# Kernel optimization log

Measured on AMD Instinct MI355X. Metric: run time of the kernel, lower is better.

Reference implementation:

```python
import jax, jax.numpy as jnp
import numpy as np

# ---- static configuration (from init_kwargs) ----
K = 2                 # kernel_size -> (2K+1)^2 = 25 window offsets
WIN = 2 * K + 1       # 5
A = WIN * WIN         # 25 window slots (ir_in replicated A times)
MUL_IN = 16           # multiplicity of each input irrep (16x0e + 16x1e)
MUL_OUT = 32          # 32x0e + 32x1e
SH0 = float(1.0 / (2.0 * np.sqrt(np.pi)))       # Y_l=0, e3nn 'integral' norm
SH1 = float(np.sqrt(3.0 / (4.0 * np.pi)))       # Y_l=1 scale (normalize=False)
CG_110 = float(1.0 / np.sqrt(3.0))              # CG for 1x1 -> 0 (dot/sqrt3)
CG_111 = float(1.0 / np.sqrt(2.0))              # CG for 1x1 -> 1 (cross/sqrt2)
# path normalization: out irrep gets 1/sqrt(fan_in) with fan = n_paths * mul_u
A0 = float(1.0 / np.sqrt(2 * A * MUL_IN))       # 0e fed by paths (0e,0e)+(1e,1e) per slot
A1 = float(1.0 / np.sqrt(3 * A * MUL_IN))       # 1e fed by (0e,1e)+(1e,0e)+(1e,1e)


def setup_inputs() -> dict:
    key = jax.random.key(0)
    ks = jax.random.split(key, 7)
    feat = jax.random.normal(ks[0], (8, 64, 64, 64), dtype=jnp.float32)
    spin = jax.random.normal(ks[1], (8, 64, 64, 3), dtype=jnp.float32)
    wshape = (A, MUL_IN, MUL_OUT)  # one uvw block per window slot per path type
    W_000 = jax.random.normal(ks[2], wshape, dtype=jnp.float32)
    W_110 = jax.random.normal(ks[3], wshape, dtype=jnp.float32)
    W_011 = jax.random.normal(ks[4], wshape, dtype=jnp.float32)
    W_101 = jax.random.normal(ks[5], wshape, dtype=jnp.float32)
    W_111 = jax.random.normal(ks[6], wshape, dtype=jnp.float32)
    return {"feat": feat, "spin": spin, "W_000": W_000, "W_110": W_110,
            "W_011": W_011, "W_101": W_101, "W_111": W_111}


def spin2colsq2d(feat):
    # circular im2col: (N,Lx,Ly,F) -> (N,Lx,Ly,A,F)
    N, Lx, Ly, F = feat.shape
    p = jnp.pad(feat, ((0, 0), (K, K), (K, K), (0, 0)), mode='wrap')
    cols = [p[:, ix:ix + Lx, iy:iy + Ly, :]
            for ix in range(WIN) for iy in range(WIN)]
    return jnp.stack(cols, axis=3)


def reference(feat, spin, W_000, W_110, W_011, W_101, W_111):
    col = spin2colsq2d(feat)                                  # (N,Lx,Ly,A,64)
    x0 = col[..., :MUL_IN]                                    # (N,Lx,Ly,A,16) scalars
    x1 = col[..., MUL_IN:].reshape(col.shape[:-1] + (MUL_IN, 3))  # (N,Lx,Ly,A,16,3)
    # spherical harmonics of spin, l=0..1, normalize=False, integral norm
    sh1 = SH1 * spin                                          # (N,Lx,Ly,3)
    # ---- paths into 0e output ----
    dot = jnp.einsum('nxyaui,nxyi->nxyau', x1, sh1) * CG_110  # 1e x 1e -> 0e
    out0 = A0 * (SH0 * jnp.einsum('nxyau,auw->nxyw', x0, W_000)
                 + jnp.einsum('nxyau,auw->nxyw', dot, W_110))  # (N,Lx,Ly,32)
    # ---- paths into 1e output ----
    cross = jnp.cross(x1, sh1[..., None, None, :]) * CG_111   # 1e x 1e -> 1e
    out1 = A1 * (jnp.einsum('nxyau,nxyi,auw->nxywi', x0, sh1, W_011)
                 + SH0 * jnp.einsum('nxyaui,auw->nxywi', x1, W_101)
                 + jnp.einsum('nxyaui,auw->nxywi', cross, W_111))  # (N,Lx,Ly,32,3)
    out1 = out1.reshape(out1.shape[:-2] + (MUL_OUT * 3,))
    return jnp.concatenate([out0, out1], axis=-1)             # (N,Lx,Ly,128)
```

## Files before the change

kernel.cpp:

```cpp
#include <hip/hip_runtime.h>


typedef __attribute__((ext_vector_type(8))) short short8;
typedef __attribute__((ext_vector_type(16))) float f32x16;
typedef __attribute__((ext_vector_type(4))) float float4v;

typedef __attribute__((address_space(3))) unsigned char lds_u8_t;
typedef const __attribute__((address_space(1))) unsigned char g_u8_t;

#define FEATT_BYTES (8u * 64u * 64u * 64u * 2u)
#define BT_OFFSET   FEATT_BYTES

#define MFMA32(A, B, C) __builtin_amdgcn_mfma_f32_32x32x16_bf16(A, B, C, 0, 0, 0)

__device__ __forceinline__ unsigned short f2bf(float f) {
    unsigned int u = __float_as_uint(f);
    return (unsigned short)((u + 0x7FFFu + ((u >> 16) & 1u)) >> 16);
}

__global__ __launch_bounds__(256) void prep_kernel(
    const float* __restrict__ feat,
    const float* __restrict__ W000, const float* __restrict__ W110,
    const float* __restrict__ W011, const float* __restrict__ W101,
    const float* __restrict__ W111,
    unsigned char* __restrict__ ws)
{
    int tid = threadIdx.x;
    int b = blockIdx.x;
    if (b < 512) {
        __shared__ float sf[64][68];
        size_t base = (size_t)b * 4096;
        #pragma unroll
        for (int i = 0; i < 4; ++i) {
            int e = tid + i * 256;
            float4v v = *(const float4v*)(feat + base + (size_t)e * 4);
            int px = e >> 4;
            int c  = (e & 15) * 4;
            sf[px][c + 0] = v[0]; sf[px][c + 1] = v[1];
            sf[px][c + 2] = v[2]; sf[px][c + 3] = v[3];
        }
        __syncthreads();
        unsigned short* dst = (unsigned short*)ws + base;
        #pragma unroll
        for (int i = 0; i < 2; ++i) {
            int t = tid + i * 256;
            int s = t >> 6, px = t & 63;
            short8 o;
            #pragma unroll
            for (int j = 0; j < 8; ++j) {
                int chp = s * 8 + j;
                int c = (chp < 16) ? chp : (16 + 3 * ((chp - 16) & 15) + ((chp - 16) >> 4));
                o[j] = (short)f2bf(sf[px][c]);
            }
            *(short8*)(dst + s * 512 + px * 8) = o;
        }
    } else {
        int t = (b - 512) * 256 + tid;
        if (t >= 4000) return;
        int a = t / 160, colv = t - a * 160;
        int arr = colv >> 5, w = colv & 31;
        const float* Wp = (arr == 0) ? W000 : (arr == 1) ? W011
                        : (arr == 2) ? W110 : (arr == 3) ? W101 : W111;
        unsigned short tmp[16];
        #pragma unroll
        for (int k = 0; k < 16; ++k) tmp[k] = f2bf(Wp[a * 512 + k * 32 + w]);
        unsigned short* d = (unsigned short*)(ws + BT_OFFSET) + (size_t)t * 16;
        *(short8*)(d)     = *(short8*)(tmp);
        *(short8*)(d + 8) = *(short8*)(tmp + 8);
    }
}

__global__ __launch_bounds__(256, 3) void spinconv_mfma_kernel(
    const unsigned char* __restrict__ featT8,
    const unsigned char* __restrict__ bt,
    const float* __restrict__ spin,
    float* __restrict__ out)
{
    const float SH0f   = 0.28209479177387814f;
    const float CG110f = 0.5773502691896258f;
    const float CG111f = 0.7071067811865476f;
    const float A0f    = 0.035355339059327376f;
    const float A1f    = 0.028867513459481287f;

    __shared__ __align__(16) unsigned char fl[5 * 8 * 64 * 16];
    __shared__ float sbuf[2][16][64];
    __shared__ float s_lds[192];

    int tid = threadIdx.x;
    int b = blockIdx.x;
    int bid = ((b & 7) << 6) + (b >> 3);
    int x = bid & 63;

    int lane = tid & 63;
    int wv4 = tid >> 6;

    #pragma unroll
    for (int i = 0; i < 10; ++i) {
        int g = wv4 * 10 + i;
        int dx = g >> 3;
        int X = (x + dx + 62) & 63;
        const unsigned char* src = featT8
            + (size_t)(bid - x + X) * 8192 + (g & 7) * 1024 + lane * 16;
        __builtin_amdgcn_global_load_lds((g_u8_t*)src, (lds_u8_t*)(fl + g * 1024), 16, 0, 0);
    }
    if (tid < 192) {
        s_lds[tid] = 0.4886025119029199f * spin[(size_t)bid * 192 + tid];
    }
    __syncthreads();

    int pair = wv4 >> 1;
    int role = wv4 & 1;
    int col = lane & 31;
    int khalf = lane >> 5;
    int yb = pair << 5;
    int p0 = bid << 6;

    const unsigned char* bbase = bt + col * 32 + khalf * 16;
    float* rowbuf = (float*)fl;

    f32x16 zz;
    #pragma unroll
    for (int i = 0; i < 16; ++i) zz[i] = 0.f;

    f32x16 aS000 = zz, aS011 = zz, aV0 = zz, aV1 = zz, aV2 = zz;
    f32x16 aT0 = zz, aT1 = zz, aT2 = zz, aU0 = zz, aU1 = zz, aU2 = zz;

    if (role == 0) {
        short8 Bc0, Bc1, Bc2, Bn0, Bn1, Bn2;
        short8 Ax, Ac0, Ac1, Ac2, Nx, Nc0, Nc1, Nc2;

        auto loadB = [&](int a, short8& b0, short8& b1, short8& b2) {
            const unsigned char* p = bbase + a * 5120;
            b0 = *(const short8*)(p);
            b1 = *(const short8*)(p + 1024);
            b2 = *(const short8*)(p + 2048);
        };
        auto loadA = [&](int a, short8& ax, short8& c0, short8& c1, short8& c2) {
            int ix = a / 5;
            int iy = a - ix * 5;
            int yn = (yb + col + iy + 62) & 63;
            const unsigned char* ab = fl + ix * 8192 + yn * 16;
            ax = *(const short8*)(ab + (0 + khalf) * 1024);
            c0 = *(const short8*)(ab + (2 + khalf) * 1024);
            c1 = *(const short8*)(ab + (4 + khalf) * 1024);
            c2 = *(const short8*)(ab + (6 + khalf) * 1024);
        };

        loadB(0, Bc0, Bc1, Bc2);
        loadA(0, Ax, Ac0, Ac1, Ac2);
        #pragma unroll
        for (int ap = 0; ap < 25; ap += 2) {
            if (ap + 1 < 25) { loadB(ap + 1, Bn0, Bn1, Bn2); loadA(ap + 1, Nx, Nc0, Nc1, Nc2); }
            __builtin_amdgcn_s_setprio(1);
            aS000 = MFMA32(Ax,  Bc0, aS000);
            aS011 = MFMA32(Ax,  Bc1, aS011);
            aV0   = MFMA32(Ac0, Bc2, aV0);
            aV1   = MFMA32(Ac1, Bc2, aV1);
            aV2   = MFMA32(Ac2, Bc2, aV2);
            __builtin_amdgcn_s_setprio(0);
            if (ap + 1 < 25) {
                if (ap + 2 < 25) { loadB(ap + 2, Bc0, Bc1, Bc2); loadA(ap + 2, Ax, Ac0, Ac1, Ac2); }
                __builtin_amdgcn_s_setprio(1);
                aS000 = MFMA32(Nx,  Bn0, aS000);
                aS011 = MFMA32(Nx,  Bn1, aS011);
                aV0   = MFMA32(Nc0, Bn2, aV0);
                aV1   = MFMA32(Nc1, Bn2, aV1);
                aV2   = MFMA32(Nc2, Bn2, aV2);
                __builtin_amdgcn_s_setprio(0);
            }
        }
        #pragma unroll
        for (int r = 0; r < 16; ++r) sbuf[pair][r][lane] = aS011[r];
    } else {
        short8 Bc0, Bc1, Bn0, Bn1;
        short8 Ac0, Ac1, Ac2, Nc0, Nc1, Nc2;

        auto loadB = [&](int a, short8& b0, short8& b1) {
            const unsigned char* p = bbase + a * 5120;
            b0 = *(const short8*)(p + 3072);
            b1 = *(const short8*)(p + 4096);
        };
        auto loadA = [&](int a, short8& c0, short8& c1, short8& c2) {
            int ix = a / 5;
            int iy = a - ix * 5;
            int yn = (yb + col + iy + 62) & 63;
            const unsigned char* ab = fl + ix * 8192 + yn * 16;
            c0 = *(const short8*)(ab + (2 + khalf) * 1024);
            c1 = *(const short8*)(ab + (4 + khalf) * 1024);
            c2 = *(const short8*)(ab + (6 + khalf) * 1024);
        };

        loadB(0, Bc0, Bc1);
        loadA(0, Ac0, Ac1, Ac2);
        #pragma unroll
        for (int ap = 0; ap < 25; ap += 2) {
            if (ap + 1 < 25) { loadB(ap + 1, Bn0, Bn1); loadA(ap + 1, Nc0, Nc1, Nc2); }
            __builtin_amdgcn_s_setprio(1);
            aT0 = MFMA32(Ac0, Bc0, aT0);
            aU0 = MFMA32(Ac0, Bc1, aU0);
            aT1 = MFMA32(Ac1, Bc0, aT1);
            aU1 = MFMA32(Ac1, Bc1, aU1);
            aT2 = MFMA32(Ac2, Bc0, aT2);
            aU2 = MFMA32(Ac2, Bc1, aU2);
            __builtin_amdgcn_s_setprio(0);
            if (ap + 1 < 25) {
                if (ap + 2 < 25) { loadB(ap + 2, Bc0, Bc1); loadA(ap + 2, Ac0, Ac1, Ac2); }
                __builtin_amdgcn_s_setprio(1);
                aT0 = MFMA32(Nc0, Bn0, aT0);
                aU0 = MFMA32(Nc0, Bn1, aU0);
                aT1 = MFMA32(Nc1, Bn0, aT1);
                aU1 = MFMA32(Nc1, Bn1, aU1);
                aT2 = MFMA32(Nc2, Bn0, aT2);
                aU2 = MFMA32(Nc2, Bn1, aU2);
                __builtin_amdgcn_s_setprio(0);
            }
        }
    }

    __syncthreads();

    if (role == 0) {
        #pragma unroll
        for (int r = 0; r < 16; ++r) {
            int row = (r & 3) + ((r >> 2) << 3) + (khalf << 2);
            int y = yb + row;
            float s0 = s_lds[y * 3 + 0];
            float s1 = s_lds[y * 3 + 1];
            float s2 = s_lds[y * 3 + 2];
            float o0 = A0f * (SH0f * aS000[r]
                     + CG110f * (s0 * aV0[r] + s1 * aV1[r] + s2 * aV2[r]));
            rowbuf[y * 128 + col] = o0;
        }
    } else {
        #pragma unroll
        for (int r = 0; r < 16; ++r) {
            int row = (r & 3) + ((r >> 2) << 3) + (khalf << 2);
            int y = yb + row;
            float s0 = s_lds[y * 3 + 0];
            float s1 = s_lds[y * 3 + 1];
            float s2 = s_lds[y * 3 + 2];
            float S011 = sbuf[pair][r][lane];
            float T0 = aT0[r], T1 = aT1[r], T2 = aT2[r];
            float U0 = aU0[r], U1 = aU1[r], U2 = aU2[r];
            float c0 = U1 * s2 - U2 * s1;
            float c1 = U2 * s0 - U0 * s2;
            float c2 = U0 * s1 - U1 * s0;
            float* rp = rowbuf + y * 128 + 32 + 3 * col;
            rp[0] = A1f * (s0 * S011 + SH0f * T0 + CG111f * c0);
            rp[1] = A1f * (s1 * S011 + SH0f * T1 + CG111f * c1);
            rp[2] = A1f * (s2 * S011 + SH0f * T2 + CG111f * c2);
        }
    }

    __syncthreads();

    float* ob = out + (size_t)p0 * 128;
    #pragma unroll
    for (int i = 0; i < 8; ++i) {
        int e = (tid + (i << 8)) << 2;
        *(float4v*)(ob + e) = *(const float4v*)(rowbuf + e);
    }
}

extern "C" void kernel_launch(void* const* d_in, const int* in_sizes, int n_in,
                              void* d_out, int out_size, void* d_ws, size_t ws_size,
                              hipStream_t stream) {
    const float* feat = (const float*)d_in[0];
    const float* spin = (const float*)d_in[1];
    const float* W000 = (const float*)d_in[2];
    const float* W110 = (const float*)d_in[3];
    const float* W011 = (const float*)d_in[4];
    const float* W101 = (const float*)d_in[5];
    const float* W111 = (const float*)d_in[6];
    float* out = (float*)d_out;
    unsigned char* ws = (unsigned char*)d_ws;

    hipLaunchKernelGGL(prep_kernel, dim3(528), dim3(256), 0, stream,
                       feat, W000, W110, W011, W101, W111, ws);
    hipLaunchKernelGGL(spinconv_mfma_kernel, dim3(512), dim3(256), 0, stream,
                       ws, ws + BT_OFFSET, spin, out);
}
```

Before: 22.76 us.

## Rebalance MFMA work between wave roles and alternate role assignment per block

Redistributes the matrix products so one wave of each pair handles the scalar-channel and first vector-component products, and the other handles the remaining two components. This gives five versus six MFMAs per slot instead of five versus six with unequal A loads, and removes the sbuf LDS exchange of S011. Roles are swapped on odd blocks, and the epilogue becomes two phases where the second wave accumulates into the row buffer after an extra barrier. Launch bounds drop from 3 to 2 blocks per SM, which allows more registers per thread but may lower occupancy.

```diff
diff --git a/kernel.cpp b/kernel.cpp
--- a/kernel.cpp
+++ b/kernel.cpp
@@ -70,7 +70,7 @@
     }
 }
 
-__global__ __launch_bounds__(256, 3) void spinconv_mfma_kernel(
+__global__ __launch_bounds__(256, 2) void spinconv_mfma_kernel(
     const unsigned char* __restrict__ featT8,
     const unsigned char* __restrict__ bt,
     const float* __restrict__ spin,
@@ -83,7 +83,6 @@
     const float A1f    = 0.028867513459481287f;
 
     __shared__ __align__(16) unsigned char fl[5 * 8 * 64 * 16];
-    __shared__ float sbuf[2][16][64];
     __shared__ float s_lds[192];
 
     int tid = threadIdx.x;
@@ -109,7 +108,7 @@
     __syncthreads();
 
     int pair = wv4 >> 1;
-    int role = wv4 & 1;
+    int role = (wv4 & 1) ^ (bid & 1);
     int col = lane & 31;
     int khalf = lane >> 5;
     int yb = pair << 5;
@@ -122,96 +121,93 @@
     #pragma unroll
     for (int i = 0; i < 16; ++i) zz[i] = 0.f;
 
-    f32x16 aS000 = zz, aS011 = zz, aV0 = zz, aV1 = zz, aV2 = zz;
-    f32x16 aT0 = zz, aT1 = zz, aT2 = zz, aU0 = zz, aU1 = zz, aU2 = zz;
+    f32x16 ac0 = zz, ac1 = zz, ac2 = zz, ac3 = zz, ac4 = zz, ac5 = zz;
 
     if (role == 0) {
-        short8 Bc0, Bc1, Bc2, Bn0, Bn1, Bn2;
-        short8 Ax, Ac0, Ac1, Ac2, Nx, Nc0, Nc1, Nc2;
-
-        auto loadB = [&](int a, short8& b0, short8& b1, short8& b2) {
+        short8 B0c, B1c, B2c, B3c, B4c, B0n, B1n, B2n, B3n, B4n;
+        short8 Axc, C0c, Axn, C0n;
+
+        auto loadB = [&](int a, short8& b0, short8& b1, short8& b2, short8& b3, short8& b4) {
             const unsigned char* p = bbase + a * 5120;
             b0 = *(const short8*)(p);
             b1 = *(const short8*)(p + 1024);
             b2 = *(const short8*)(p + 2048);
-        };
-        auto loadA = [&](int a, short8& ax, short8& c0, short8& c1, short8& c2) {
+            b3 = *(const short8*)(p + 3072);
+            b4 = *(const short8*)(p + 4096);
+        };
+        auto loadA = [&](int a, short8& ax, short8& c0) {
             int ix = a / 5;
             int iy = a - ix * 5;
             int yn = (yb + col + iy + 62) & 63;
             const unsigned char* ab = fl + ix * 8192 + yn * 16;
             ax = *(const short8*)(ab + (0 + khalf) * 1024);
             c0 = *(const short8*)(ab + (2 + khalf) * 1024);
-            c1 = *(const short8*)(ab + (4 + khalf) * 1024);
-            c2 = *(const short8*)(ab + (6 + khalf) * 1024);
-        };
-
-        loadB(0, Bc0, Bc1, Bc2);
-        loadA(0, Ax, Ac0, Ac1, Ac2);
+        };
+
+        loadB(0, B0c, B1c, B2c, B3c, B4c);
+        loadA(0, Axc, C0c);
         #pragma unroll
         for (int ap = 0; ap < 25; ap += 2) {
-            if (ap + 1 < 25) { loadB(ap + 1, Bn0, Bn1, Bn2); loadA(ap + 1, Nx, Nc0, Nc1, Nc2); }
+            if (ap + 1 < 25) { loadB(ap + 1, B0n, B1n, B2n, B3n, B4n); loadA(ap + 1, Axn, C0n); }
             __builtin_amdgcn_s_setprio(1);
-            aS000 = MFMA32(Ax,  Bc0, aS000);
-            aS011 = MFMA32(Ax,  Bc1, aS011);
-            aV0   = MFMA32(Ac0, Bc2, aV0);
-            aV1   = MFMA32(Ac1, Bc2, aV1);
-            aV2   = MFMA32(Ac2, Bc2, aV2);
+            ac0 = MFMA32(Axc, B0c, ac0);
+            ac1 = MFMA32(Axc, B1c, ac1);
+            ac2 = MFMA32(C0c, B2c, ac2);
+            ac3 = MFMA32(C0c, B3c, ac3);
+            ac4 = MFMA32(C0c, B4c, ac4);
             __builtin_amdgcn_s_setprio(0);
             if (ap + 1 < 25) {
-                if (ap + 2 < 25) { loadB(ap + 2, Bc0, Bc1, Bc2); loadA(ap + 2, Ax, Ac0, Ac1, Ac2); }
+                if (ap + 2 < 25) { loadB(ap + 2, B0c, B1c, B2c, B3c, B4c); loadA(ap + 2, Axc, C0c); }
                 __builtin_amdgcn_s_setprio(1);
-                aS000 = MFMA32(Nx,  Bn0, aS000);
-                aS011 = MFMA32(Nx,  Bn1, aS011);
-                aV0   = MFMA32(Nc0, Bn2, aV0);
-                aV1   = MFMA32(Nc1, Bn2, aV1);
-                aV2   = MFMA32(Nc2, Bn2, aV2);
+                ac0 = MFMA32(Axn, B0n, ac0);
+                ac1 = MFMA32(Axn, B1n, ac1);
+                ac2 = MFMA32(C0n, B2n, ac2);
+                ac3 = MFMA32(C0n, B3n, ac3);
+                ac4 = MFMA32(C0n, B4n, ac4);
                 __builtin_amdgcn_s_setprio(0);
             }
         }
-        #pragma unroll
-        for (int r = 0; r < 16; ++r) sbuf[pair][r][lane] = aS011[r];
     } else {
-        short8 Bc0, Bc1, Bn0, Bn1;
-        short8 Ac0, Ac1, Ac2, Nc0, Nc1, Nc2;
-
-        auto loadB = [&](int a, short8& b0, short8& b1) {
+        short8 B2c, B3c, B4c, B2n, B3n, B4n;
+        short8 C1c, C2c, C1n, C2n;
+
+        auto loadB = [&](int a, short8& b2, short8& b3, short8& b4) {
             const unsigned char* p = bbase + a * 5120;
-            b0 = *(const short8*)(p + 3072);
-            b1 = *(const short8*)(p + 4096);
-        };
-        auto loadA = [&](int a, short8& c0, short8& c1, short8& c2) {
+            b2 = *(const short8*)(p + 2048);
+            b3 = *(const short8*)(p + 3072);
+            b4 = *(const short8*)(p + 4096);
+        };
+        auto loadA = [&](int a, short8& c1, short8& c2) {
             int ix = a / 5;
             int iy = a - ix * 5;
             int yn = (yb + col + iy + 62) & 63;
             const unsigned char* ab = fl + ix * 8192 + yn * 16;
-            c0 = *(const short8*)(ab + (2 + khalf) * 1024);
             c1 = *(const short8*)(ab + (4 + khalf) * 1024);
             c2 = *(const short8*)(ab + (6 + khalf) * 1024);
         };
 
-        loadB(0, Bc0, Bc1);
-        loadA(0, Ac0, Ac1, Ac2);
+        loadB(0, B2c, B3c, B4c);
+        loadA(0, C1c, C2c);
         #pragma unroll
         for (int ap = 0; ap < 25; ap += 2) {
-            if (ap + 1 < 25) { loadB(ap + 1, Bn0, Bn1); loadA(ap + 1, Nc0, Nc1, Nc2); }
+            if (ap + 1 < 25) { loadB(ap + 1, B2n, B3n, B4n); loadA(ap + 1, C1n, C2n); }
             __builtin_amdgcn_s_setprio(1);
-            aT0 = MFMA32(Ac0, Bc0, aT0);
-            aU0 = MFMA32(Ac0, Bc1, aU0);
-            aT1 = MFMA32(Ac1, Bc0, aT1);
-            aU1 = MFMA32(Ac1, Bc1, aU1);
-            aT2 = MFMA32(Ac2, Bc0, aT2);
-            aU2 = MFMA32(Ac2, Bc1, aU2);
+            ac0 = MFMA32(C1c, B2c, ac0);
+            ac1 = MFMA32(C2c, B2c, ac1);
+            ac2 = MFMA32(C1c, B3c, ac2);
+            ac3 = MFMA32(C2c, B3c, ac3);
+            ac4 = MFMA32(C1c, B4c, ac4);
+            ac5 = MFMA32(C2c, B4c, ac5);
             __builtin_amdgcn_s_setprio(0);
             if (ap + 1 < 25) {
-                if (ap + 2 < 25) { loadB(ap + 2, Bc0, Bc1); loadA(ap + 2, Ac0, Ac1, Ac2); }
+                if (ap + 2 < 25) { loadB(ap + 2, B2c, B3c, B4c); loadA(ap + 2, C1c, C2c); }
                 __builtin_amdgcn_s_setprio(1);
-                aT0 = MFMA32(Nc0, Bn0, aT0);
-                aU0 = MFMA32(Nc0, Bn1, aU0);
-                aT1 = MFMA32(Nc1, Bn0, aT1);
-                aU1 = MFMA32(Nc1, Bn1, aU1);
-                aT2 = MFMA32(Nc2, Bn0, aT2);
-                aU2 = MFMA32(Nc2, Bn1, aU2);
+                ac0 = MFMA32(C1n, B2n, ac0);
+                ac1 = MFMA32(C2n, B2n, ac1);
+                ac2 = MFMA32(C1n, B3n, ac2);
+                ac3 = MFMA32(C2n, B3n, ac3);
+                ac4 = MFMA32(C1n, B4n, ac4);
+                ac5 = MFMA32(C2n, B4n, ac5);
                 __builtin_amdgcn_s_setprio(0);
             }
         }
@@ -227,11 +223,17 @@
             float s0 = s_lds[y * 3 + 0];
             float s1 = s_lds[y * 3 + 1];
             float s2 = s_lds[y * 3 + 2];
-            float o0 = A0f * (SH0f * aS000[r]
-                     + CG110f * (s0 * aV0[r] + s1 * aV1[r] + s2 * aV2[r]));
-            rowbuf[y * 128 + col] = o0;
-        }
-    } else {
+            float S000 = ac0[r], S011 = ac1[r];
+            float V0 = ac2[r], T0 = ac3[r], U0 = ac4[r];
+            rowbuf[y * 128 + col] = A0f * (SH0f * S000 + CG110f * s0 * V0);
+            float* rp = rowbuf + y * 128 + 32 + 3 * col;
+            rp[0] = A1f * (s0 * S011 + SH0f * T0);
+            rp[1] = A1f * (s1 * S011 - CG111f * U0 * s2);
+            rp[2] = A1f * (s2 * S011 + CG111f * U0 * s1);
+        }
+    }
+    __syncthreads();
+    if (role == 1) {
         #pragma unroll
         for (int r = 0; r < 16; ++r) {
             int row = (r & 3) + ((r >> 2) << 3) + (khalf << 2);
@@ -239,19 +241,16 @@
             float s0 = s_lds[y * 3 + 0];
             float s1 = s_lds[y * 3 + 1];
             float s2 = s_lds[y * 3 + 2];
-            float S011 = sbuf[pair][r][lane];
-            float T0 = aT0[r], T1 = aT1[r], T2 = aT2[r];
-            float U0 = aU0[r], U1 = aU1[r], U2 = aU2[r];
-            float c0 = U1 * s2 - U2 * s1;
-            float c1 = U2 * s0 - U0 * s2;
-            float c2 = U0 * s1 - U1 * s0;
+            float V1 = ac0[r], V2 = ac1[r];
+            float T1 = ac2[r], T2 = ac3[r];
+            float U1 = ac4[r], U2 = ac5[r];
+            rowbuf[y * 128 + col] += A0f * CG110f * (s1 * V1 + s2 * V2);
             float* rp = rowbuf + y * 128 + 32 + 3 * col;
-            rp[0] = A1f * (s0 * S011 + SH0f * T0 + CG111f * c0);
-            rp[1] = A1f * (s1 * S011 + SH0f * T1 + CG111f * c1);
-            rp[2] = A1f * (s2 * S011 + SH0f * T2 + CG111f * c2);
-        }
-    }
-
+            rp[0] += A1f * CG111f * (U1 * s2 - U2 * s1);
+            rp[1] += A1f * (SH0f * T1 + CG111f * U2 * s0);
+            rp[2] += A1f * (SH0f * T2 - CG111f * U1 * s0);
+        }
+    }
     __syncthreads();
 
     float* ob = out + (size_t)p0 * 128;
```

Result: slower. 24.80 us (+9.0%).
